# Kernel tuning notes

Measured on AMD Instinct MI355X. Metric: run time of the kernel, lower is better.

The kernel has to match this reference:

```python
import jax, jax.numpy as jnp
import numpy as np

N_HEADS = 8
TANH_CLIP = 10.0


def setup_inputs() -> dict:
    key = jax.random.key(0)
    ks = jax.random.split(key, 7)
    B, N, D = 128, 1000, 512
    embeddings = jax.random.normal(ks[0], (B, N, D), dtype=jnp.float32)
    step_context = jax.random.normal(ks[1], (B, 1, 2 * D), dtype=jnp.float32)
    # action mask: True = feasible action; guarantee at least one feasible per row
    action_mask = jax.random.uniform(ks[2], (B, 1, N)) > 0.3
    action_mask = action_mask.at[:, :, 0].set(True)
    s = 0.02
    W_node = jax.random.normal(ks[3], (D, 3 * D), dtype=jnp.float32) * s
    W_fixed = jax.random.normal(ks[4], (D, D), dtype=jnp.float32) * s
    W_step = jax.random.normal(ks[5], (2 * D, D), dtype=jnp.float32) * s
    W_out = jax.random.normal(ks[6], (D, D), dtype=jnp.float32) * s
    return {"embeddings": embeddings, "step_context": step_context,
            "action_mask": action_mask, "W_node": W_node, "W_fixed": W_fixed,
            "W_step": W_step, "W_out": W_out}


def reference(embeddings, step_context, action_mask, W_node, W_fixed, W_step, W_out):
    B, N, D = embeddings.shape
    H = N_HEADS
    hd = D // H
    neg_inf = jnp.float32(-jnp.inf)

    # --- precompute (Decoder._precompute) ---
    graph_embed = embeddings.mean(axis=1)                      # [B, D]
    kvl = embeddings @ W_node                                  # [B, N, 3D]
    _gk, gv, logit_key = jnp.split(kvl, 3, axis=-1)
    # source bug: glimpse_key variable is overwritten with glimpse_val, and
    # attention is called with key = value = glimpse_val
    KV = gv.reshape(B, N, H, hd).transpose(0, 2, 1, 3)         # [B, H, N, hd]
    graph_context = (graph_embed @ W_fixed)[:, None, :]        # [B, 1, D]

    # --- per-step query (Decoder._get_log_p) ---
    query = graph_context + step_context @ W_step              # [B, 1, D]
    q = query.reshape(B, 1, H, hd).transpose(0, 2, 1, 3)       # [B, H, 1, hd]

    # --- inner MHA (scaled_dot_product_attention with boolean mask) ---
    scores = jnp.einsum('bhqs,bhns->bhqn', q, KV) / jnp.sqrt(jnp.float32(hd))
    scores = jnp.where(action_mask[:, None, :, :], scores, neg_inf)  # [B,H,1,N]
    attn = jax.nn.softmax(scores, axis=-1)
    heads = jnp.einsum('bhqn,bhns->bhqs', attn, KV)            # [B, H, 1, hd]
    heads = heads.transpose(0, 2, 1, 3).reshape(B, 1, D)       # [B, 1, D]

    # --- glimpse projection and logit head ---
    glimpse = heads @ W_out                                    # [B, 1, D]
    logits = jnp.einsum('bqd,bnd->bqn', glimpse, logit_key) / jnp.sqrt(jnp.float32(D))
    logits = jnp.tanh(logits) * TANH_CLIP
    logits = jnp.where(action_mask, logits, neg_inf)
    return jax.nn.log_softmax(logits, axis=-1)                 # [B, 1, N]
```

## Files before the change

kernel.cpp:

```cpp
#include <hip/hip_runtime.h>
#include <math.h>

#define B 128
#define N 1000
#define D 512
#define H 8
#define NCH 8
#define CHK 125
#define NCHM 20
#define CHKM 50
#define WPB 4

#define OFF_PMEAN 0
#define OFF_QW    (OFF_PMEAN + B*NCHM*D)
#define OFF_PAE   (OFF_QW + B*D*H)
#define OFF_ZC    (OFF_PAE + B*NCH*H*D)
#define OFF_GW    (OFF_ZC + B*NCH*H)
#define OFF_LG    (OFF_GW + B*D)
#define OFF_LMAX  (OFF_LG + B*N)
#define OFF_LSUM  (OFF_LMAX + B*NCH)

__global__ void k1_partial_mean(const float* __restrict__ emb, float* __restrict__ ws){
    int chunk = blockIdx.x, b = blockIdx.y, t = threadIdx.x;
    const float4* e4 = (const float4*)emb + ((size_t)b * N + (size_t)chunk * CHKM) * (D / 4) + t;
    float4 acc = make_float4(0.f, 0.f, 0.f, 0.f);
    #pragma unroll 2
    for (int n = 0; n < CHKM; ++n) {
        float4 v = e4[(size_t)n * (D / 4)];
        acc.x += v.x; acc.y += v.y; acc.z += v.z; acc.w += v.w;
    }
    ((float4*)(ws + OFF_PMEAN + (size_t)(b * NCHM + chunk) * D))[t] = acc;
}

__global__ void k2_prep(const float* __restrict__ stepc, const float* __restrict__ Wnode,
                        const float* __restrict__ Wfix, const float* __restrict__ Wstep,
                        float* __restrict__ ws){
    int b = blockIdx.x, d = threadIdx.x;
    __shared__ float ge[D];
    __shared__ float q[D];
    float s = 0.f;
    #pragma unroll
    for (int c = 0; c < NCHM; ++c) s += ws[OFF_PMEAN + (size_t)(b * NCHM + c) * D + d];
    ge[d] = s * (1.0f / N);
    __syncthreads();
    float a0 = 0.f, a1 = 0.f, a2 = 0.f, a3 = 0.f;
    for (int k = 0; k < D; k += 4) {
        a0 = fmaf(ge[k],     Wfix[(size_t)k * D + d],       a0);
        a1 = fmaf(ge[k + 1], Wfix[(size_t)(k + 1) * D + d], a1);
        a2 = fmaf(ge[k + 2], Wfix[(size_t)(k + 2) * D + d], a2);
        a3 = fmaf(ge[k + 3], Wfix[(size_t)(k + 3) * D + d], a3);
    }
    const float* sc = stepc + (size_t)b * 2 * D;
    for (int k = 0; k < 2 * D; k += 4) {
        a0 = fmaf(sc[k],     Wstep[(size_t)k * D + d],       a0);
        a1 = fmaf(sc[k + 1], Wstep[(size_t)(k + 1) * D + d], a1);
        a2 = fmaf(sc[k + 2], Wstep[(size_t)(k + 2) * D + d], a2);
        a3 = fmaf(sc[k + 3], Wstep[(size_t)(k + 3) * D + d], a3);
    }
    q[d] = (a0 + a1) + (a2 + a3);
    __syncthreads();
    const float* wrow = Wnode + (size_t)d * 3 * D + D;
    float* outp = ws + OFF_QW + ((size_t)b * D + d) * H;
    #pragma unroll
    for (int h = 0; h < H; ++h) {
        float a = 0.f;
        const float* qh = q + h * 64;
        const float* wh = wrow + h * 64;
        #pragma unroll 8
        for (int s2 = 0; s2 < 64; ++s2) a = fmaf(qh[s2], wh[s2], a);
        outp[h] = a;
    }
}

__global__ __launch_bounds__(256) void kb_attn(const float* __restrict__ emb,
        const unsigned char* __restrict__ mask, float* __restrict__ ws){
    const int cg = blockIdx.x, b = blockIdx.y, t = threadIdx.x;
    const int w = t >> 6, l = t & 63;
    __shared__ float p_lds[128][H];
    float4 qv[16];
    {
        const float4* q4 = (const float4*)(ws + OFF_QW + (size_t)b * D * H) + l * 16;
        #pragma unroll
        for (int j = 0; j < 16; ++j) qv[j] = q4[j];
    }
    const float* embb = emb + ((size_t)b * N + (size_t)cg * CHK) * D;
    const unsigned char* mb = mask + (size_t)b * N + cg * CHK;
    for (int nl = w; nl < CHK; nl += WPB) {
        const float4* er = (const float4*)(embb + (size_t)nl * D) + l * 2;
        float4 e0 = er[0], e1 = er[1];
        float part[8];
        #pragma unroll
        for (int h = 0; h < 8; ++h) part[h] = 0.f;
#define ACCJ(j, ev) { \
        part[0] = fmaf(ev, qv[2*(j)].x, part[0]); part[1] = fmaf(ev, qv[2*(j)].y, part[1]); \
        part[2] = fmaf(ev, qv[2*(j)].z, part[2]); part[3] = fmaf(ev, qv[2*(j)].w, part[3]); \
        part[4] = fmaf(ev, qv[2*(j)+1].x, part[4]); part[5] = fmaf(ev, qv[2*(j)+1].y, part[5]); \
        part[6] = fmaf(ev, qv[2*(j)+1].z, part[6]); part[7] = fmaf(ev, qv[2*(j)+1].w, part[7]); }
        ACCJ(0, e0.x) ACCJ(1, e0.y) ACCJ(2, e0.z) ACCJ(3, e0.w)
        ACCJ(4, e1.x) ACCJ(5, e1.y) ACCJ(6, e1.z) ACCJ(7, e1.w)
#undef ACCJ
        #pragma unroll
        for (int o = 32; o > 0; o >>= 1) {
            #pragma unroll
            for (int h = 0; h < 8; ++h) part[h] += __shfl_xor(part[h], o);
        }
        bool m = mb[nl] != 0;
        float pe[8];
        #pragma unroll
        for (int h = 0; h < 8; ++h) pe[h] = m ? __expf(part[h] * 0.125f) : 0.f;
        if (l == 0) {
            *(float4*)&p_lds[nl][0] = make_float4(pe[0], pe[1], pe[2], pe[3]);
            *(float4*)&p_lds[nl][4] = make_float4(pe[4], pe[5], pe[6], pe[7]);
        }
    }
    __syncthreads();
    if (t < H) {
        float z = 0.f;
        for (int i = 0; i < CHK; ++i) z += p_lds[i][t];
        ws[OFF_ZC + ((size_t)b * NCH + cg) * H + t] = z;
    }
    {
        float2 acc[8];
        #pragma unroll
        for (int h = 0; h < 8; ++h) acc[h] = make_float2(0.f, 0.f);
        const float2* ecol = (const float2*)embb + t;
        #pragma unroll 2
        for (int i = 0; i < CHK; ++i) {
            float2 e = ecol[(size_t)i * (D / 2)];
            float4 pa = *(const float4*)&p_lds[i][0];
            float4 pb = *(const float4*)&p_lds[i][4];
            acc[0].x = fmaf(pa.x, e.x, acc[0].x); acc[0].y = fmaf(pa.x, e.y, acc[0].y);
            acc[1].x = fmaf(pa.y, e.x, acc[1].x); acc[1].y = fmaf(pa.y, e.y, acc[1].y);
            acc[2].x = fmaf(pa.z, e.x, acc[2].x); acc[2].y = fmaf(pa.z, e.y, acc[2].y);
            acc[3].x = fmaf(pa.w, e.x, acc[3].x); acc[3].y = fmaf(pa.w, e.y, acc[3].y);
            acc[4].x = fmaf(pb.x, e.x, acc[4].x); acc[4].y = fmaf(pb.x, e.y, acc[4].y);
            acc[5].x = fmaf(pb.y, e.x, acc[5].x); acc[5].y = fmaf(pb.y, e.y, acc[5].y);
            acc[6].x = fmaf(pb.z, e.x, acc[6].x); acc[6].y = fmaf(pb.z, e.y, acc[6].y);
            acc[7].x = fmaf(pb.w, e.x, acc[7].x); acc[7].y = fmaf(pb.w, e.y, acc[7].y);
        }
        float2* paeb = (float2*)(ws + OFF_PAE) + ((size_t)(b * NCH + cg) * H) * (D / 2) + t;
        #pragma unroll
        for (int h = 0; h < 8; ++h) paeb[(size_t)h * (D / 2)] = acc[h];
    }
}

__global__ __launch_bounds__(512) void kd_post(const float* __restrict__ Wnode,
        const float* __restrict__ Wout, float* __restrict__ ws){
    int b = blockIdx.x, t = threadIdx.x;
    __shared__ float ae[H * D];
    __shared__ float heads[D];
    __shared__ float gl[D];
    __shared__ float iZ[H];
    if (t < H) {
        float Z = 0.f;
        #pragma unroll
        for (int c = 0; c < NCH; ++c)
            Z += ws[OFF_ZC + ((size_t)b * NCH + c) * H + t];
        iZ[t] = 1.0f / Z;
    }
    __syncthreads();
    #pragma unroll
    for (int h = 0; h < H; ++h) {
        float s = 0.f;
        #pragma unroll
        for (int c = 0; c < NCH; ++c)
            s += ws[OFF_PAE + (((size_t)b * NCH + c) * H + h) * (size_t)D + t];
        ae[h * D + t] = s * iZ[h];
    }
    __syncthreads();
    {
        int h = t >> 6;
        const float* aeh = ae + h * D;
        const float* col = Wnode + 512 + t;
        float a0 = 0.f, a1 = 0.f, a2 = 0.f, a3 = 0.f;
        for (int d = 0; d < D; d += 4) {
            a0 = fmaf(aeh[d],     col[(size_t)d * (3 * D)],       a0);
            a1 = fmaf(aeh[d + 1], col[(size_t)(d + 1) * (3 * D)], a1);
            a2 = fmaf(aeh[d + 2], col[(size_t)(d + 2) * (3 * D)], a2);
            a3 = fmaf(aeh[d + 3], col[(size_t)(d + 3) * (3 * D)], a3);
        }
        heads[t] = (a0 + a1) + (a2 + a3);
    }
    __syncthreads();
    {
        float a0 = 0.f, a1 = 0.f, a2 = 0.f, a3 = 0.f;
        for (int d = 0; d < D; d += 4) {
            a0 = fmaf(heads[d],     Wout[(size_t)d * D + t],       a0);
            a1 = fmaf(heads[d + 1], Wout[(size_t)(d + 1) * D + t], a1);
            a2 = fmaf(heads[d + 2], Wout[(size_t)(d + 2) * D + t], a2);
            a3 = fmaf(heads[d + 3], Wout[(size_t)(d + 3) * D + t], a3);
        }
        gl[t] = (a0 + a1) + (a2 + a3);
    }
    __syncthreads();
    {
        const float* wrow = Wnode + (size_t)t * (3 * D) + 2 * D;
        float a0 = 0.f, a1 = 0.f, a2 = 0.f, a3 = 0.f;
        for (int e = 0; e < D; e += 4) {
            a0 = fmaf(gl[e],     wrow[e],     a0);
            a1 = fmaf(gl[e + 1], wrow[e + 1], a1);
            a2 = fmaf(gl[e + 2], wrow[e + 2], a2);
            a3 = fmaf(gl[e + 3], wrow[e + 3], a3);
        }
        ws[OFF_GW + (size_t)b * D + t] = (a0 + a1) + (a2 + a3);
    }
}

__global__ __launch_bounds__(256) void kc_logits(const float* __restrict__ emb,
        const unsigned char* __restrict__ mask, float* __restrict__ ws){
    const int cg = blockIdx.x, b = blockIdx.y, t = threadIdx.x;
    const int w = t >> 6, l = t & 63;
    __shared__ float wm[WPB], wsum[WPB];
    float4 g0, g1;
    {
        const float4* g4 = (const float4*)(ws + OFF_GW + (size_t)b * D) + l * 2;
        g0 = g4[0]; g1 = g4[1];
    }
    const float* embb = emb + ((size_t)b * N + (size_t)cg * CHK) * D;
    const unsigned char* mb = mask + (size_t)b * N + cg * CHK;
    float m = -INFINITY, s = 0.f;
    for (int nl = w; nl < CHK; nl += WPB) {
        const float4* er = (const float4*)(embb + (size_t)nl * D) + l * 2;
        float4 e0 = er[0], e1 = er[1];
        float a0 = fmaf(e0.x, g0.x, 0.f), a1 = fmaf(e0.y, g0.y, 0.f);
        float a2 = fmaf(e0.z, g0.z, 0.f), a3 = fmaf(e0.w, g0.w, 0.f);
        a0 = fmaf(e1.x, g1.x, a0); a1 = fmaf(e1.y, g1.y, a1);
        a2 = fmaf(e1.z, g1.z, a2); a3 = fmaf(e1.w, g1.w, a3);
        float a = (a0 + a1) + (a2 + a3);
        #pragma unroll
        for (int o = 32; o > 0; o >>= 1) a += __shfl_xor(a, o);
        bool mk = mb[nl] != 0;
        float lg = mk ? tanhf(a * 0.044194173824159216f) * 10.0f : -INFINITY;
        if (l == 0) ws[OFF_LG + (size_t)b * N + cg * CHK + nl] = lg;
        if (lg != -INFINITY) {
            float mn = fmaxf(m, lg);
            s = s * __expf(m - mn) + __expf(lg - mn);
            m = mn;
        }
    }
    if (l == 0) { wm[w] = m; wsum[w] = s; }
    __syncthreads();
    if (t == 0) {
        float M = -INFINITY;
        #pragma unroll
        for (int i = 0; i < WPB; ++i) M = fmaxf(M, wm[i]);
        float S = 0.f;
        #pragma unroll
        for (int i = 0; i < WPB; ++i)
            if (wm[i] != -INFINITY) S += wsum[i] * __expf(wm[i] - M);
        ws[OFF_LMAX + (size_t)b * NCH + cg] = M;
        ws[OFF_LSUM + (size_t)b * NCH + cg] = S;
    }
}

__global__ void k8_out(const float* __restrict__ ws, float* __restrict__ out){
    int b = blockIdx.x, t = threadIdx.x;
    __shared__ float Ls;
    if (t == 0) {
        float M = -INFINITY;
        #pragma unroll
        for (int c = 0; c < NCH; ++c)
            M = fmaxf(M, ws[OFF_LMAX + (size_t)b * NCH + c]);
        float S = 0.f;
        #pragma unroll
        for (int c = 0; c < NCH; ++c) {
            float m = ws[OFF_LMAX + (size_t)b * NCH + c];
            if (m != -INFINITY) S += __expf(m - M) * ws[OFF_LSUM + (size_t)b * NCH + c];
        }
        Ls = M + __logf(S);
    }
    __syncthreads();
    float L = Ls;
    for (int j = t; j < N; j += 256)
        out[(size_t)b * N + j] = fmaxf(ws[OFF_LG + (size_t)b * N + j] - L, -1e30f);
}

extern "C" void kernel_launch(void* const* d_in, const int* in_sizes, int n_in,
                              void* d_out, int out_size, void* d_ws, size_t ws_size,
                              hipStream_t stream) {
    const float* emb   = (const float*)d_in[0];
    const float* stepc = (const float*)d_in[1];
    const unsigned char* mask = (const unsigned char*)d_in[2];
    const float* Wnode = (const float*)d_in[3];
    const float* Wfix  = (const float*)d_in[4];
    const float* Wstep = (const float*)d_in[5];
    const float* Wout  = (const float*)d_in[6];
    float* out = (float*)d_out;
    float* ws  = (float*)d_ws;

    k1_partial_mean<<<dim3(NCHM, B), 128, 0, stream>>>(emb, ws);
    k2_prep<<<dim3(B), 512, 0, stream>>>(stepc, Wnode, Wfix, Wstep, ws);
    kb_attn<<<dim3(NCH, B), 256, 0, stream>>>(emb, mask, ws);
    kd_post<<<dim3(B), 512, 0, stream>>>(Wnode, Wout, ws);
    kc_logits<<<dim3(NCH, B), 256, 0, stream>>>(emb, mask, ws);
    k8_out<<<dim3(B), 256, 0, stream>>>(ws, out);
}
```

Before: 390.4 us.

## Split attention score work across 8 waves by head pair, relayout Q

```diff
diff --git a/kernel.cpp b/kernel.cpp
--- a/kernel.cpp
+++ b/kernel.cpp
@@ -9,7 +9,6 @@
 #define CHK 125
 #define NCHM 20
 #define CHKM 50
-#define WPB 4
 
 #define OFF_PMEAN 0
 #define OFF_QW    (OFF_PMEAN + B*NCHM*D)
@@ -60,7 +59,6 @@
     q[d] = (a0 + a1) + (a2 + a3);
     __syncthreads();
     const float* wrow = Wnode + (size_t)d * 3 * D + D;
-    float* outp = ws + OFF_QW + ((size_t)b * D + d) * H;
     #pragma unroll
     for (int h = 0; h < H; ++h) {
         float a = 0.f;
@@ -68,49 +66,49 @@
         const float* wh = wrow + h * 64;
         #pragma unroll 8
         for (int s2 = 0; s2 < 64; ++s2) a = fmaf(qh[s2], wh[s2], a);
-        outp[h] = a;
-    }
-}
-
-__global__ __launch_bounds__(256) void kb_attn(const float* __restrict__ emb,
+        ws[OFF_QW + ((size_t)b * H + h) * D + d] = a;
+    }
+}
+
+__global__ __launch_bounds__(512, 2) void kb_attn(const float* __restrict__ emb,
         const unsigned char* __restrict__ mask, float* __restrict__ ws){
     const int cg = blockIdx.x, b = blockIdx.y, t = threadIdx.x;
     const int w = t >> 6, l = t & 63;
-    __shared__ float p_lds[128][H];
-    float4 qv[16];
-    {
-        const float4* q4 = (const float4*)(ws + OFF_QW + (size_t)b * D * H) + l * 16;
-        #pragma unroll
-        for (int j = 0; j < 16; ++j) qv[j] = q4[j];
+    const int hp = w & 3, half = w >> 2;
+    __shared__ float p_lds[CHK][H];
+    float4 qa0, qa1, qb0, qb1;
+    {
+        const float4* qA = (const float4*)(ws + OFF_QW + ((size_t)b * H + 2 * hp) * D) + l * 2;
+        const float4* qB = (const float4*)(ws + OFF_QW + ((size_t)b * H + 2 * hp + 1) * D) + l * 2;
+        qa0 = qA[0]; qa1 = qA[1]; qb0 = qB[0]; qb1 = qB[1];
     }
     const float* embb = emb + ((size_t)b * N + (size_t)cg * CHK) * D;
     const unsigned char* mb = mask + (size_t)b * N + cg * CHK;
-    for (int nl = w; nl < CHK; nl += WPB) {
+    const int r0 = half * 63, r1 = half ? CHK : 63;
+    for (int nl = r0; nl < r1; ++nl) {
         const float4* er = (const float4*)(embb + (size_t)nl * D) + l * 2;
         float4 e0 = er[0], e1 = er[1];
-        float part[8];
-        #pragma unroll
-        for (int h = 0; h < 8; ++h) part[h] = 0.f;
-#define ACCJ(j, ev) { \
-        part[0] = fmaf(ev, qv[2*(j)].x, part[0]); part[1] = fmaf(ev, qv[2*(j)].y, part[1]); \
-        part[2] = fmaf(ev, qv[2*(j)].z, part[2]); part[3] = fmaf(ev, qv[2*(j)].w, part[3]); \
-        part[4] = fmaf(ev, qv[2*(j)+1].x, part[4]); part[5] = fmaf(ev, qv[2*(j)+1].y, part[5]); \
-        part[6] = fmaf(ev, qv[2*(j)+1].z, part[6]); part[7] = fmaf(ev, qv[2*(j)+1].w, part[7]); }
-        ACCJ(0, e0.x) ACCJ(1, e0.y) ACCJ(2, e0.z) ACCJ(3, e0.w)
-        ACCJ(4, e1.x) ACCJ(5, e1.y) ACCJ(6, e1.z) ACCJ(7, e1.w)
-#undef ACCJ
+        float pA0 = 0.f, pA1 = 0.f, pB0 = 0.f, pB1 = 0.f;
+        pA0 = fmaf(e0.x, qa0.x, pA0); pA1 = fmaf(e0.y, qa0.y, pA1);
+        pA0 = fmaf(e0.z, qa0.z, pA0); pA1 = fmaf(e0.w, qa0.w, pA1);
+        pA0 = fmaf(e1.x, qa1.x, pA0); pA1 = fmaf(e1.y, qa1.y, pA1);
+        pA0 = fmaf(e1.z, qa1.z, pA0); pA1 = fmaf(e1.w, qa1.w, pA1);
+        pB0 = fmaf(e0.x, qb0.x, pB0); pB1 = fmaf(e0.y, qb0.y, pB1);
+        pB0 = fmaf(e0.z, qb0.z, pB0); pB1 = fmaf(e0.w, qb0.w, pB1);
+        pB0 = fmaf(e1.x, qb1.x, pB0); pB1 = fmaf(e1.y, qb1.y, pB1);
+        pB0 = fmaf(e1.z, qb1.z, pB0); pB1 = fmaf(e1.w, qb1.w, pB1);
+        float vA = pA0 + pA1, vB = pB0 + pB1;
         #pragma unroll
         for (int o = 32; o > 0; o >>= 1) {
-            #pragma unroll
-            for (int h = 0; h < 8; ++h) part[h] += __shfl_xor(part[h], o);
-        }
-        bool m = mb[nl] != 0;
-        float pe[8];
-        #pragma unroll
-        for (int h = 0; h < 8; ++h) pe[h] = m ? __expf(part[h] * 0.125f) : 0.f;
+            vA += __shfl_xor(vA, o);
+            vB += __shfl_xor(vB, o);
+        }
         if (l == 0) {
-            *(float4*)&p_lds[nl][0] = make_float4(pe[0], pe[1], pe[2], pe[3]);
-            *(float4*)&p_lds[nl][4] = make_float4(pe[4], pe[5], pe[6], pe[7]);
+            bool m = mb[nl] != 0;
+            float2 pe;
+            pe.x = m ? __expf(vA * 0.125f) : 0.f;
+            pe.y = m ? __expf(vB * 0.125f) : 0.f;
+            *(float2*)&p_lds[nl][2 * hp] = pe;
         }
     }
     __syncthreads();
@@ -120,27 +118,23 @@
         ws[OFF_ZC + ((size_t)b * NCH + cg) * H + t] = z;
     }
     {
-        float2 acc[8];
-        #pragma unroll
-        for (int h = 0; h < 8; ++h) acc[h] = make_float2(0.f, 0.f);
-        const float2* ecol = (const float2*)embb + t;
+        float acc[H];
+        #pragma unroll
+        for (int h = 0; h < H; ++h) acc[h] = 0.f;
+        const float* ecol = embb + t;
         #pragma unroll 2
         for (int i = 0; i < CHK; ++i) {
-            float2 e = ecol[(size_t)i * (D / 2)];
+            float e = ecol[(size_t)i * D];
             float4 pa = *(const float4*)&p_lds[i][0];
             float4 pb = *(const float4*)&p_lds[i][4];
-            acc[0].x = fmaf(pa.x, e.x, acc[0].x); acc[0].y = fmaf(pa.x, e.y, acc[0].y);
-            acc[1].x = fmaf(pa.y, e.x, acc[1].x); acc[1].y = fmaf(pa.y, e.y, acc[1].y);
-            acc[2].x = fmaf(pa.z, e.x, acc[2].x); acc[2].y = fmaf(pa.z, e.y, acc[2].y);
-            acc[3].x = fmaf(pa.w, e.x, acc[3].x); acc[3].y = fmaf(pa.w, e.y, acc[3].y);
-            acc[4].x = fmaf(pb.x, e.x, acc[4].x); acc[4].y = fmaf(pb.x, e.y, acc[4].y);
-            acc[5].x = fmaf(pb.y, e.x, acc[5].x); acc[5].y = fmaf(pb.y, e.y, acc[5].y);
-            acc[6].x = fmaf(pb.z, e.x, acc[6].x); acc[6].y = fmaf(pb.z, e.y, acc[6].y);
-            acc[7].x = fmaf(pb.w, e.x, acc[7].x); acc[7].y = fmaf(pb.w, e.y, acc[7].y);
-        }
-        float2* paeb = (float2*)(ws + OFF_PAE) + ((size_t)(b * NCH + cg) * H) * (D / 2) + t;
-        #pragma unroll
-        for (int h = 0; h < 8; ++h) paeb[(size_t)h * (D / 2)] = acc[h];
+            acc[0] = fmaf(pa.x, e, acc[0]); acc[1] = fmaf(pa.y, e, acc[1]);
+            acc[2] = fmaf(pa.z, e, acc[2]); acc[3] = fmaf(pa.w, e, acc[3]);
+            acc[4] = fmaf(pb.x, e, acc[4]); acc[5] = fmaf(pb.y, e, acc[5]);
+            acc[6] = fmaf(pb.z, e, acc[6]); acc[7] = fmaf(pb.w, e, acc[7]);
+        }
+        float* paeb = ws + OFF_PAE + (((size_t)b * NCH + cg) * H) * (size_t)D + t;
+        #pragma unroll
+        for (int h = 0; h < H; ++h) paeb[(size_t)h * D] = acc[h];
     }
 }
 
@@ -206,11 +200,11 @@
     }
 }
 
-__global__ __launch_bounds__(256) void kc_logits(const float* __restrict__ emb,
+__global__ __launch_bounds__(512, 2) void kc_logits(const float* __restrict__ emb,
         const unsigned char* __restrict__ mask, float* __restrict__ ws){
     const int cg = blockIdx.x, b = blockIdx.y, t = threadIdx.x;
     const int w = t >> 6, l = t & 63;
-    __shared__ float wm[WPB], wsum[WPB];
+    __shared__ float wm[8], wsum[8];
     float4 g0, g1;
     {
         const float4* g4 = (const float4*)(ws + OFF_GW + (size_t)b * D) + l * 2;
@@ -219,20 +213,19 @@
     const float* embb = emb + ((size_t)b * N + (size_t)cg * CHK) * D;
     const unsigned char* mb = mask + (size_t)b * N + cg * CHK;
     float m = -INFINITY, s = 0.f;
-    for (int nl = w; nl < CHK; nl += WPB) {
+    for (int nl = w; nl < CHK; nl += 8) {
         const float4* er = (const float4*)(embb + (size_t)nl * D) + l * 2;
         float4 e0 = er[0], e1 = er[1];
-        float a0 = fmaf(e0.x, g0.x, 0.f), a1 = fmaf(e0.y, g0.y, 0.f);
-        float a2 = fmaf(e0.z, g0.z, 0.f), a3 = fmaf(e0.w, g0.w, 0.f);
+        float a0 = e0.x * g0.x + e0.y * g0.y, a1 = e0.z * g0.z + e0.w * g0.w;
         a0 = fmaf(e1.x, g1.x, a0); a1 = fmaf(e1.y, g1.y, a1);
-        a2 = fmaf(e1.z, g1.z, a2); a3 = fmaf(e1.w, g1.w, a3);
-        float a = (a0 + a1) + (a2 + a3);
+        a0 = fmaf(e1.z, g1.z, a0); a1 = fmaf(e1.w, g1.w, a1);
+        float a = a0 + a1;
         #pragma unroll
         for (int o = 32; o > 0; o >>= 1) a += __shfl_xor(a, o);
         bool mk = mb[nl] != 0;
         float lg = mk ? tanhf(a * 0.044194173824159216f) * 10.0f : -INFINITY;
         if (l == 0) ws[OFF_LG + (size_t)b * N + cg * CHK + nl] = lg;
-        if (lg != -INFINITY) {
+        if (mk) {
             float mn = fmaxf(m, lg);
             s = s * __expf(m - mn) + __expf(lg - mn);
             m = mn;
@@ -243,10 +236,10 @@
     if (t == 0) {
         float M = -INFINITY;
         #pragma unroll
-        for (int i = 0; i < WPB; ++i) M = fmaxf(M, wm[i]);
+        for (int i = 0; i < 8; ++i) M = fmaxf(M, wm[i]);
         float S = 0.f;
         #pragma unroll
-        for (int i = 0; i < WPB; ++i)
+        for (int i = 0; i < 8; ++i)
             if (wm[i] != -INFINITY) S += wsum[i] * __expf(wm[i] - M);
         ws[OFF_LMAX + (size_t)b * NCH + cg] = M;
         ws[OFF_LSUM + (size_t)b * NCH + cg] = S;
@@ -290,8 +283,8 @@
 
     k1_partial_mean<<<dim3(NCHM, B), 128, 0, stream>>>(emb, ws);
     k2_prep<<<dim3(B), 512, 0, stream>>>(stepc, Wnode, Wfix, Wstep, ws);
-    kb_attn<<<dim3(NCH, B), 256, 0, stream>>>(emb, mask, ws);
+    kb_attn<<<dim3(NCH, B), 512, 0, stream>>>(emb, mask, ws);
     kd_post<<<dim3(B), 512, 0, stream>>>(Wnode, Wout, ws);
-    kc_logits<<<dim3(NCH, B), 256, 0, stream>>>(emb, mask, ws);
+    kc_logits<<<dim3(NCH, B), 512, 0, stream>>>(emb, mask, ws);
     k8_out<<<dim3(B), 256, 0, stream>>>(ws, out);
 }
```

After: 404.9 us. 1.04x slower.

## Retile attention/logit passes with coalesced row loads and head-major query layout

Applied to the files above, without the earlier changes.

```diff
diff --git a/kernel.cpp b/kernel.cpp
--- a/kernel.cpp
+++ b/kernel.cpp
@@ -5,30 +5,47 @@
 #define N 1000
 #define D 512
 #define H 8
-#define NCH 8
-#define CHK 125
-#define NCHM 20
-#define CHKM 50
-#define WPB 4
-
-#define OFF_PMEAN 0
-#define OFF_QW    (OFF_PMEAN + B*NCHM*D)
-#define OFF_PAE   (OFF_QW + B*D*H)
+#define NCH 10
+#define CHK 100
+#define NCHM 25
+#define CHKM 40
+
+#define OFF_QW    0
+#define OFF_PMEAN (OFF_QW + B*H*D)
+#define OFF_PAE   OFF_PMEAN
 #define OFF_ZC    (OFF_PAE + B*NCH*H*D)
 #define OFF_GW    (OFF_ZC + B*NCH*H)
 #define OFF_LG    (OFF_GW + B*D)
 #define OFF_LMAX  (OFF_LG + B*N)
 #define OFF_LSUM  (OFF_LMAX + B*NCH)
 
+__device__ inline float dot4(float4 a, float4 b){
+    float r = a.x * b.x;
+    r = fmaf(a.y, b.y, r);
+    r = fmaf(a.z, b.z, r);
+    r = fmaf(a.w, b.w, r);
+    return r;
+}
+
 __global__ void k1_partial_mean(const float* __restrict__ emb, float* __restrict__ ws){
     int chunk = blockIdx.x, b = blockIdx.y, t = threadIdx.x;
     const float4* e4 = (const float4*)emb + ((size_t)b * N + (size_t)chunk * CHKM) * (D / 4) + t;
-    float4 acc = make_float4(0.f, 0.f, 0.f, 0.f);
-    #pragma unroll 2
-    for (int n = 0; n < CHKM; ++n) {
-        float4 v = e4[(size_t)n * (D / 4)];
-        acc.x += v.x; acc.y += v.y; acc.z += v.z; acc.w += v.w;
-    }
+    float4 a0 = make_float4(0,0,0,0), a1 = a0, a2 = a0, a3 = a0;
+    for (int n = 0; n < CHKM; n += 4) {
+        float4 v0 = e4[(size_t)(n + 0) * (D / 4)];
+        float4 v1 = e4[(size_t)(n + 1) * (D / 4)];
+        float4 v2 = e4[(size_t)(n + 2) * (D / 4)];
+        float4 v3 = e4[(size_t)(n + 3) * (D / 4)];
+        a0.x += v0.x; a0.y += v0.y; a0.z += v0.z; a0.w += v0.w;
+        a1.x += v1.x; a1.y += v1.y; a1.z += v1.z; a1.w += v1.w;
+        a2.x += v2.x; a2.y += v2.y; a2.z += v2.z; a2.w += v2.w;
+        a3.x += v3.x; a3.y += v3.y; a3.z += v3.z; a3.w += v3.w;
+    }
+    float4 acc;
+    acc.x = (a0.x + a1.x) + (a2.x + a3.x);
+    acc.y = (a0.y + a1.y) + (a2.y + a3.y);
+    acc.z = (a0.z + a1.z) + (a2.z + a3.z);
+    acc.w = (a0.w + a1.w) + (a2.w + a3.w);
     ((float4*)(ws + OFF_PMEAN + (size_t)(b * NCHM + chunk) * D))[t] = acc;
 }
 
@@ -60,7 +77,6 @@
     q[d] = (a0 + a1) + (a2 + a3);
     __syncthreads();
     const float* wrow = Wnode + (size_t)d * 3 * D + D;
-    float* outp = ws + OFF_QW + ((size_t)b * D + d) * H;
     #pragma unroll
     for (int h = 0; h < H; ++h) {
         float a = 0.f;
@@ -68,49 +84,53 @@
         const float* wh = wrow + h * 64;
         #pragma unroll 8
         for (int s2 = 0; s2 < 64; ++s2) a = fmaf(qh[s2], wh[s2], a);
-        outp[h] = a;
-    }
-}
-
-__global__ __launch_bounds__(256) void kb_attn(const float* __restrict__ emb,
+        ws[OFF_QW + ((size_t)b * H + h) * D + d] = a;
+    }
+}
+
+__global__ __launch_bounds__(256, 4) void kb_attn(const float* __restrict__ emb,
         const unsigned char* __restrict__ mask, float* __restrict__ ws){
     const int cg = blockIdx.x, b = blockIdx.y, t = threadIdx.x;
     const int w = t >> 6, l = t & 63;
-    __shared__ float p_lds[128][H];
-    float4 qv[16];
-    {
-        const float4* q4 = (const float4*)(ws + OFF_QW + (size_t)b * D * H) + l * 16;
-        #pragma unroll
-        for (int j = 0; j < 16; ++j) qv[j] = q4[j];
+    __shared__ float p_lds[CHK][H];
+    float4 qlo[H], qhi[H];
+    {
+        const float* qb = ws + OFF_QW + (size_t)b * H * D;
+        #pragma unroll
+        for (int h = 0; h < H; ++h) {
+            qlo[h] = *(const float4*)(qb + (size_t)h * D + 4 * l);
+            qhi[h] = *(const float4*)(qb + (size_t)h * D + 256 + 4 * l);
+        }
     }
     const float* embb = emb + ((size_t)b * N + (size_t)cg * CHK) * D;
     const unsigned char* mb = mask + (size_t)b * N + cg * CHK;
-    for (int nl = w; nl < CHK; nl += WPB) {
-        const float4* er = (const float4*)(embb + (size_t)nl * D) + l * 2;
-        float4 e0 = er[0], e1 = er[1];
-        float part[8];
-        #pragma unroll
-        for (int h = 0; h < 8; ++h) part[h] = 0.f;
-#define ACCJ(j, ev) { \
-        part[0] = fmaf(ev, qv[2*(j)].x, part[0]); part[1] = fmaf(ev, qv[2*(j)].y, part[1]); \
-        part[2] = fmaf(ev, qv[2*(j)].z, part[2]); part[3] = fmaf(ev, qv[2*(j)].w, part[3]); \
-        part[4] = fmaf(ev, qv[2*(j)+1].x, part[4]); part[5] = fmaf(ev, qv[2*(j)+1].y, part[5]); \
-        part[6] = fmaf(ev, qv[2*(j)+1].z, part[6]); part[7] = fmaf(ev, qv[2*(j)+1].w, part[7]); }
-        ACCJ(0, e0.x) ACCJ(1, e0.y) ACCJ(2, e0.z) ACCJ(3, e0.w)
-        ACCJ(4, e1.x) ACCJ(5, e1.y) ACCJ(6, e1.z) ACCJ(7, e1.w)
-#undef ACCJ
+    for (int i = 0; i < CHK / 4; ++i) {
+        const int nl = 4 * i + w;
+        const float4* er = (const float4*)(embb + (size_t)nl * D) + l;
+        float4 e0 = er[0];
+        float4 e1 = er[64];
+        float s[H];
+        #pragma unroll
+        for (int h = 0; h < H; ++h)
+            s[h] = dot4(e0, qlo[h]) + dot4(e1, qhi[h]);
         #pragma unroll
         for (int o = 32; o > 0; o >>= 1) {
             #pragma unroll
-            for (int h = 0; h < 8; ++h) part[h] += __shfl_xor(part[h], o);
-        }
-        bool m = mb[nl] != 0;
-        float pe[8];
-        #pragma unroll
-        for (int h = 0; h < 8; ++h) pe[h] = m ? __expf(part[h] * 0.125f) : 0.f;
+            for (int h = 0; h < H; ++h) s[h] += __shfl_xor(s[h], o);
+        }
         if (l == 0) {
-            *(float4*)&p_lds[nl][0] = make_float4(pe[0], pe[1], pe[2], pe[3]);
-            *(float4*)&p_lds[nl][4] = make_float4(pe[4], pe[5], pe[6], pe[7]);
+            bool m = mb[nl] != 0;
+            float4 p0, p1;
+            p0.x = m ? __expf(s[0] * 0.125f) : 0.f;
+            p0.y = m ? __expf(s[1] * 0.125f) : 0.f;
+            p0.z = m ? __expf(s[2] * 0.125f) : 0.f;
+            p0.w = m ? __expf(s[3] * 0.125f) : 0.f;
+            p1.x = m ? __expf(s[4] * 0.125f) : 0.f;
+            p1.y = m ? __expf(s[5] * 0.125f) : 0.f;
+            p1.z = m ? __expf(s[6] * 0.125f) : 0.f;
+            p1.w = m ? __expf(s[7] * 0.125f) : 0.f;
+            *(float4*)&p_lds[nl][0] = p0;
+            *(float4*)&p_lds[nl][4] = p1;
         }
     }
     __syncthreads();
@@ -120,9 +140,9 @@
         ws[OFF_ZC + ((size_t)b * NCH + cg) * H + t] = z;
     }
     {
-        float2 acc[8];
-        #pragma unroll
-        for (int h = 0; h < 8; ++h) acc[h] = make_float2(0.f, 0.f);
+        float2 acc[H];
+        #pragma unroll
+        for (int h = 0; h < H; ++h) acc[h] = make_float2(0.f, 0.f);
         const float2* ecol = (const float2*)embb + t;
         #pragma unroll 2
         for (int i = 0; i < CHK; ++i) {
@@ -140,7 +160,7 @@
         }
         float2* paeb = (float2*)(ws + OFF_PAE) + ((size_t)(b * NCH + cg) * H) * (D / 2) + t;
         #pragma unroll
-        for (int h = 0; h < 8; ++h) paeb[(size_t)h * (D / 2)] = acc[h];
+        for (int h = 0; h < H; ++h) paeb[(size_t)h * (D / 2)] = acc[h];
     }
 }
 
@@ -206,33 +226,32 @@
     }
 }
 
-__global__ __launch_bounds__(256) void kc_logits(const float* __restrict__ emb,
+__global__ __launch_bounds__(256, 4) void kc_logits(const float* __restrict__ emb,
         const unsigned char* __restrict__ mask, float* __restrict__ ws){
     const int cg = blockIdx.x, b = blockIdx.y, t = threadIdx.x;
     const int w = t >> 6, l = t & 63;
-    __shared__ float wm[WPB], wsum[WPB];
-    float4 g0, g1;
-    {
-        const float4* g4 = (const float4*)(ws + OFF_GW + (size_t)b * D) + l * 2;
-        g0 = g4[0]; g1 = g4[1];
+    __shared__ float wm[4], wsum[4];
+    float4 glo, ghi;
+    {
+        const float* gb = ws + OFF_GW + (size_t)b * D;
+        glo = *(const float4*)(gb + 4 * l);
+        ghi = *(const float4*)(gb + 256 + 4 * l);
     }
     const float* embb = emb + ((size_t)b * N + (size_t)cg * CHK) * D;
     const unsigned char* mb = mask + (size_t)b * N + cg * CHK;
     float m = -INFINITY, s = 0.f;
-    for (int nl = w; nl < CHK; nl += WPB) {
-        const float4* er = (const float4*)(embb + (size_t)nl * D) + l * 2;
-        float4 e0 = er[0], e1 = er[1];
-        float a0 = fmaf(e0.x, g0.x, 0.f), a1 = fmaf(e0.y, g0.y, 0.f);
-        float a2 = fmaf(e0.z, g0.z, 0.f), a3 = fmaf(e0.w, g0.w, 0.f);
-        a0 = fmaf(e1.x, g1.x, a0); a1 = fmaf(e1.y, g1.y, a1);
-        a2 = fmaf(e1.z, g1.z, a2); a3 = fmaf(e1.w, g1.w, a3);
-        float a = (a0 + a1) + (a2 + a3);
+    for (int i = 0; i < CHK / 4; ++i) {
+        const int nl = 4 * i + w;
+        const float4* er = (const float4*)(embb + (size_t)nl * D) + l;
+        float4 e0 = er[0];
+        float4 e1 = er[64];
+        float a = dot4(e0, glo) + dot4(e1, ghi);
         #pragma unroll
         for (int o = 32; o > 0; o >>= 1) a += __shfl_xor(a, o);
         bool mk = mb[nl] != 0;
         float lg = mk ? tanhf(a * 0.044194173824159216f) * 10.0f : -INFINITY;
         if (l == 0) ws[OFF_LG + (size_t)b * N + cg * CHK + nl] = lg;
-        if (lg != -INFINITY) {
+        if (mk) {
             float mn = fmaxf(m, lg);
             s = s * __expf(m - mn) + __expf(lg - mn);
             m = mn;
@@ -243,10 +262,10 @@
     if (t == 0) {
         float M = -INFINITY;
         #pragma unroll
-        for (int i = 0; i < WPB; ++i) M = fmaxf(M, wm[i]);
+        for (int i = 0; i < 4; ++i) M = fmaxf(M, wm[i]);
         float S = 0.f;
         #pragma unroll
-        for (int i = 0; i < WPB; ++i)
+        for (int i = 0; i < 4; ++i)
             if (wm[i] != -INFINITY) S += wsum[i] * __expf(wm[i] - M);
         ws[OFF_LMAX + (size_t)b * NCH + cg] = M;
         ws[OFF_LSUM + (size_t)b * NCH + cg] = S;
```

Result: faster. 363.4 us (-6.9%).
